# Kernel optimization log

Hardware: AMD Instinct MI355X
Metric: run time of the kernel (lower is better)

Reference implementation:

```python
import jax, jax.numpy as jnp
import numpy as np

K_CODES = 64
EPS_LN = 1e-5


def hamilton_product(p, q):
    # p, q: [..., D] with D = 4*Q, components ordered (r, i, j, k)
    Q = p.shape[-1] // 4
    pr, pi, pj, pk = (p[..., :Q], p[..., Q:2*Q], p[..., 2*Q:3*Q], p[..., 3*Q:])
    qr, qi, qj, qk = (q[..., :Q], q[..., Q:2*Q], q[..., 2*Q:3*Q], q[..., 3*Q:])
    out_r = pr * qr - pi * qi - pj * qj - pk * qk
    out_i = pr * qi + pi * qr + pj * qk - pk * qj
    out_j = pr * qj - pi * qk + pj * qr + pk * qi
    out_k = pr * qk + pi * qj - pj * qi + pk * qr
    return jnp.concatenate([out_r, out_i, out_j, out_k], axis=-1)


def quaternion_linear(x, w4, b):
    # w4: [4, Qo, Qi] stacked (r, i, j, k); builds Hamilton block matrix [D, D]
    r, i, j, k = w4[0], w4[1], w4[2], w4[3]
    W = jnp.block([[r, -i, -j, -k],
                   [i,  r, -k,  j],
                   [j,  k,  r, -i],
                   [k, -j,  i,  r]])
    return x @ W.T + b


def quaternion_layernorm(x, gamma, beta):
    # independent LayerNorm over each quaternion component (4 chunks of size Q)
    Qd = x.shape[-1] // 4
    xs = x.reshape(*x.shape[:-1], 4, Qd)
    mu = xs.mean(axis=-1, keepdims=True)
    var = ((xs - mu) ** 2).mean(axis=-1, keepdims=True)
    xn = (xs - mu) / jnp.sqrt(var + EPS_LN)
    out = xn * gamma + beta  # gamma/beta: [4, Qd]
    return out.reshape(*x.shape[:-1], 4 * Qd)


def setup_inputs() -> dict:
    key = jax.random.key(0)
    ks = jax.random.split(key, 8)
    B, N, D, m = 8, 4096, 512, 3
    Qd = D // 4
    q = jax.random.normal(ks[0], (B, N, D), dtype=jnp.float32)
    assign_idx = jax.random.randint(ks[1], (B, N, m), 0, K_CODES)
    assign_w = jax.random.uniform(ks[2], (B, N, m), dtype=jnp.float32)
    contribute_mask = jnp.ones((B, N), dtype=jnp.float32)
    scale = 0.5 / np.sqrt(Qd)
    proto_w = jax.random.normal(ks[3], (4, Qd, Qd), dtype=jnp.float32) * scale
    proto_b = jax.random.normal(ks[4], (D,), dtype=jnp.float32) * 0.01
    upd_w = jax.random.normal(ks[5], (4, Qd, Qd), dtype=jnp.float32) * scale
    upd_b = jax.random.normal(ks[6], (D,), dtype=jnp.float32) * 0.01
    ln_gamma = jnp.ones((4, Qd), dtype=jnp.float32)
    ln_beta = jnp.zeros((4, Qd), dtype=jnp.float32)
    return {"q": q, "assign_idx": assign_idx, "assign_w": assign_w,
            "contribute_mask": contribute_mask, "proto_w": proto_w,
            "proto_b": proto_b, "upd_w": upd_w, "upd_b": upd_b,
            "ln_gamma": ln_gamma, "ln_beta": ln_beta}


def reference(q, assign_idx, assign_w, contribute_mask, proto_w, proto_b,
              upd_w, upd_b, ln_gamma, ln_beta):
    B, N, D = q.shape
    m = assign_idx.shape[-1]
    K = K_CODES

    # --- scatter-add prototype aggregation ---
    agg_w = assign_w * contribute_mask[..., None]            # [B, N, m]
    flat_idx = assign_idx.reshape(B, N * m)                  # [B, N*m]
    flat_w = agg_w.reshape(B, N * m, 1)                      # [B, N*m, 1]
    weighted_q = (q[:, :, None, :] * agg_w[..., None]).reshape(B, N * m, D)

    seg = lambda v, idx: jax.ops.segment_sum(v, idx, num_segments=K)
    proto = jax.vmap(seg)(weighted_q, flat_idx)              # [B, K, D]
    weight_sum = jax.vmap(seg)(flat_w, flat_idx)             # [B, K, 1]
    proto = proto / (weight_sum + 1e-6)
    proto = quaternion_linear(proto, proto_w, proto_b)       # [B, K, D]

    # --- gather prototypes per observation + Hamilton routing ---
    proto_per_obs = jax.vmap(lambda p, idx: p[idx])(proto, assign_idx)  # [B, N, m, D]
    routed = hamilton_product(q[:, :, None, :], proto_per_obs)          # [B, N, m, D]
    msg = (routed * assign_w[..., None]).sum(axis=2)                    # [B, N, D]
    msg = quaternion_linear(msg, upd_w, upd_b)

    q_new = quaternion_layernorm(q + msg, ln_gamma, ln_beta)
    return q_new, proto
```

## Files before the change

kernel.cpp:

```cpp
#include <hip/hip_runtime.h>
#include <hip/hip_bf16.h>

#define B_ 8
#define N_ 4096
#define D_ 512
#define K_ 64
#define QD_ 128

typedef float f32x4 __attribute__((ext_vector_type(4)));
typedef short short8 __attribute__((ext_vector_type(8)));
typedef unsigned short u16;
typedef unsigned int u32;

__device__ __forceinline__ u16 f2bf(float f) {
  u32 u = __float_as_uint(f);
  return (u16)((u + 0x7fffu + ((u >> 16) & 1u)) >> 16);
}
__device__ __forceinline__ float bf2f(u16 h) {
  return __uint_as_float((u32)h << 16);
}

__device__ __forceinline__ void load8f(const float* p, float* r) {
  float4 a = *(const float4*)(p);
  float4 b = *(const float4*)(p + 4);
  r[0] = a.x; r[1] = a.y; r[2] = a.z; r[3] = a.w;
  r[4] = b.x; r[5] = b.y; r[6] = b.z; r[7] = b.w;
}

__device__ __forceinline__ void store_comp(char* msgL, int row, int u, int s,
                                           int swz, const float* m) {
  uint4 val;
  val.x = (u32)f2bf(m[0]) | ((u32)f2bf(m[1]) << 16);
  val.y = (u32)f2bf(m[2]) | ((u32)f2bf(m[3]) << 16);
  val.z = (u32)f2bf(m[4]) | ((u32)f2bf(m[5]) << 16);
  val.w = (u32)f2bf(m[6]) | ((u32)f2bf(m[7]) << 16);
  const int byte = (row * 1024 + u * 256 + s * 16) ^ swz;
  *(uint4*)(msgL + byte) = val;
}

__global__ __launch_bounds__(256) void k_prep(
    const float* __restrict__ uw, const float* __restrict__ pw,
    u16* __restrict__ uwf, u16* __restrict__ pwf,
    const int* __restrict__ aidx, const float* __restrict__ aw,
    const float* __restrict__ mask, u16* __restrict__ A) {
  if (blockIdx.x < 2048) {
    const int gid = blockIdx.x * 256 + threadIdx.x;
    const int sel = gid >> 18;
    const int idx = gid & ((1 << 18) - 1);
    const int e = idx & 7;
    const int lane = (idx >> 3) & 63;
    const int ks = (idx >> 9) & 15;
    const int cf = idx >> 13;
    const int col = (cf >> 3) * 128 + (cf & 7) * 16 + (lane & 15);
    const int v = ks * 32 + (lane >> 4) * 8 + e;
    const int u = col >> 7, a = col & 127, c = v >> 7, bb = v & 127;
    const int   matT[4][4] = {{0,1,2,3},{1,0,3,2},{2,3,0,1},{3,2,1,0}};
    const float sgnT[4][4] = {{1.f,-1.f,-1.f,-1.f},{1.f,1.f,-1.f,1.f},
                              {1.f,1.f,1.f,-1.f},{1.f,-1.f,1.f,1.f}};
    const float* w4 = sel ? pw : uw;
    u16* dst = sel ? pwf : uwf;
    dst[idx] = f2bf(sgnT[u][c] * w4[matT[u][c] * QD_ * QD_ + a * QD_ + bb]);
  } else {
    const int gid = (blockIdx.x - 2048) * 256 + threadIdx.x;
    const int b = gid >> 12, n = gid & 4095;
    const size_t ib = (size_t)gid * 3;
    const int k0 = aidx[ib], k1 = aidx[ib + 1], k2 = aidx[ib + 2];
    const float mk = mask[gid];
    float w0 = aw[ib] * mk, w1 = aw[ib + 1] * mk, w2 = aw[ib + 2] * mk;
    bool skip1 = false, skip2 = false;
    if (k1 == k0) { w0 += w1; skip1 = true; }
    if (k2 == k0) { w0 += w2; skip2 = true; }
    else if (k2 == k1 && !skip1) { w1 += w2; skip2 = true; }
    u16* Ab = A + (size_t)b * K_ * N_;
#pragma unroll
    for (int k = 0; k < K_; ++k) Ab[(size_t)k * N_ + n] = 0;
    Ab[(size_t)k0 * N_ + n] = f2bf(w0);
    if (!skip1) Ab[(size_t)k1 * N_ + n] = f2bf(w1);
    if (!skip2) Ab[(size_t)k2 * N_ + n] = f2bf(w2);
  }
}

__global__ __launch_bounds__(256) void k_gemmA(
    const u16* __restrict__ A, const float* __restrict__ q,
    float* __restrict__ proto_raw, float* __restrict__ wsum) {
  __shared__ __align__(16) u16 Bt[128 * 64];
  const int t = threadIdx.x;
  const int bid = blockIdx.x;
  const int wg = (bid & 7) * 64 + (bid >> 3);
  const int kc = wg & 15;
  const int dq = (wg >> 4) & 3;
  const int b = wg >> 6;
  const int n_base = kc * 256;
  const u16* Ab = A + (size_t)b * K_ * N_;
  const float* qb = q + ((size_t)b * N_ + n_base) * D_ + dq * 128;

  const int lane = t & 63, wv = t >> 6;
  const int g = lane >> 4, l16 = lane & 15;
  const int sn = t >> 2, sdq = (t & 3) * 32;

  f32x4 acc[4][2];
#pragma unroll
  for (int mt = 0; mt < 4; ++mt)
#pragma unroll
    for (int nt = 0; nt < 2; ++nt) { f32x4 z = {0.f,0.f,0.f,0.f}; acc[mt][nt] = z; }

  float4 pre[8];
#pragma unroll
  for (int e = 0; e < 8; ++e)
    pre[e] = *(const float4*)(qb + (size_t)sn * D_ + sdq + e * 4);

  for (int sub = 0; sub < 4; ++sub) {
    __syncthreads();
#pragma unroll
    for (int e = 0; e < 8; ++e) {
      const float4 v = pre[e];
#pragma unroll
      for (int x = 0; x < 4; ++x) {
        const int d = sdq + e * 4 + x;
        const float fv = (x == 0) ? v.x : (x == 1) ? v.y : (x == 2) ? v.z : v.w;
        const int byte = (d * 128 + sn * 2) ^ ((d & 7) << 4);
        *(u16*)((char*)Bt + byte) = f2bf(fv);
      }
    }
    float4 nxt[8];
    if (sub < 3) {
#pragma unroll
      for (int e = 0; e < 8; ++e)
        nxt[e] = *(const float4*)(qb + (size_t)((sub + 1) * 64 + sn) * D_ + sdq + e * 4);
    }
    __syncthreads();
    const int n0 = n_base + sub * 64;
#pragma unroll
    for (int ks = 0; ks < 2; ++ks) {
      short8 bfrag[2];
#pragma unroll
      for (int nt = 0; nt < 2; ++nt) {
        const int d = wv * 32 + nt * 16 + l16;
        const int byte = (d * 128 + (ks * 32 + g * 8) * 2) ^ ((d & 7) << 4);
        bfrag[nt] = *(const short8*)((const char*)Bt + byte);
      }
#pragma unroll
      for (int mt = 0; mt < 4; ++mt) {
        const short8 afr = *(const short8*)(Ab + (size_t)(mt * 16 + l16) * N_ +
                                            n0 + ks * 32 + g * 8);
#pragma unroll
        for (int nt = 0; nt < 2; ++nt)
          acc[mt][nt] = __builtin_amdgcn_mfma_f32_16x16x32_bf16(afr, bfrag[nt], acc[mt][nt], 0, 0, 0);
      }
    }
#pragma unroll
    for (int e = 0; e < 8; ++e) pre[e] = nxt[e];
  }

#pragma unroll
  for (int mt = 0; mt < 4; ++mt)
#pragma unroll
    for (int nt = 0; nt < 2; ++nt)
#pragma unroll
      for (int rg = 0; rg < 4; ++rg) {
        const int code = mt * 16 + g * 4 + rg;
        const int d = dq * 128 + wv * 32 + nt * 16 + l16;
        atomicAdd(&proto_raw[((size_t)b * K_ + code) * D_ + d], acc[mt][nt][rg]);
      }

  if (dq == 0) {
    const int k = t >> 2, part = t & 3;
    const u16* ap = Ab + (size_t)k * N_ + n_base + part * 64;
    float s = 0.f;
#pragma unroll
    for (int i = 0; i < 8; ++i) {
      const short8 v = *(const short8*)(ap + i * 8);
#pragma unroll
      for (int e = 0; e < 8; ++e) s += bf2f((u16)v[e]);
    }
    s += __shfl_xor(s, 1);
    s += __shfl_xor(s, 2);
    if (part == 0) atomicAdd(&wsum[b * K_ + k], s);
  }
}

__global__ __launch_bounds__(256) void k_proto_mfma(
    const float* __restrict__ proto_raw, const float* __restrict__ wsum,
    const u16* __restrict__ pwf, const float* __restrict__ pb,
    float* __restrict__ proto_t, float* __restrict__ out_proto) {
  __shared__ __align__(16) u16 msgL[16 * 512];
  __shared__ float invs[16];
  const int t = threadIdx.x;
  const size_t R0 = (size_t)blockIdx.x * 16;
  if (t < 16) invs[t] = 1.f / (wsum[R0 + t] + 1e-6f);
  __syncthreads();

  {
    const int s = t & 15, row = t >> 4;
    const float iv = invs[row];
    const float* base = proto_raw + (R0 + row) * D_;
    const int swz = (row & 7) << 4;
#pragma unroll
    for (int u = 0; u < 4; ++u) {
      float m[8];
      load8f(base + u * 128 + s * 8, m);
#pragma unroll
      for (int e = 0; e < 8; ++e) m[e] *= iv;
      store_comp((char*)msgL, row, u, s, swz, m);
    }
  }
  __syncthreads();

  const int lane = t & 63, wv = t >> 6;
  const int g = lane >> 4, l16 = lane & 15;
  f32x4 acc[8];
#pragma unroll
  for (int f = 0; f < 8; ++f) { f32x4 z = {0.f,0.f,0.f,0.f}; acc[f] = z; }
#pragma unroll 4
  for (int ks = 0; ks < 16; ++ks) {
    const int arow = l16;
    const short8 a = *(const short8*)((const char*)msgL +
        ((arow * 1024 + ks * 64 + g * 16) ^ ((arow & 7) << 4)));
#pragma unroll
    for (int f = 0; f < 8; ++f) {
      const short8 bv = *(const short8*)(pwf +
          ((size_t)((wv * 8 + f) * 16 + ks) * 64 + lane) * 8);
      acc[f] = __builtin_amdgcn_mfma_f32_16x16x32_bf16(a, bv, acc[f], 0, 0, 0);
    }
  }

#pragma unroll
  for (int f = 0; f < 8; ++f) {
    const int col = wv * 128 + f * 16 + l16;
    const float pbv = pb[col];
#pragma unroll
    for (int rg = 0; rg < 4; ++rg) {
      const size_t row = R0 + g * 4 + rg;
      const float v = acc[f][rg] + pbv;
      proto_t[row * D_ + col] = v;
      out_proto[row * D_ + col] = v;
    }
  }
}

__global__ __launch_bounds__(256) void k_main8(
    const float* __restrict__ q, const int* __restrict__ aidx,
    const float* __restrict__ aw, const float* __restrict__ proto_t,
    const u16* __restrict__ uwf, const float* __restrict__ ub,
    const float* __restrict__ gamma, const float* __restrict__ beta,
    float* __restrict__ out_q) {
  __shared__ __align__(16) u16 msgL[32 * 512];
  const int t = threadIdx.x;
  const int bid = blockIdx.x;
  const size_t R0 = (size_t)((bid & 7) * 128 + (bid >> 3)) * 32;

  {
    const int s = t & 15, rowHalf = t >> 4;
    int kks[2][3]; float wws[2][3];
#pragma unroll
    for (int p = 0; p < 2; ++p) {
      const size_t gr = R0 + p * 16 + rowHalf;
      const int* ip = aidx + gr * 3;
      const float* wp = aw + gr * 3;
#pragma unroll
      for (int j = 0; j < 3; ++j) { kks[p][j] = ip[j]; wws[p][j] = wp[j]; }
    }
#pragma unroll
    for (int p = 0; p < 2; ++p) {
      const int row = p * 16 + rowHalf;
      const size_t gr = R0 + row;
      const int b = (int)(gr >> 12);
      const float* qp = q + gr * D_ + s * 8;
      float qr_[8], qi_[8], qj_[8], qk_[8];
      load8f(qp, qr_); load8f(qp + 128, qi_);
      load8f(qp + 256, qj_); load8f(qp + 384, qk_);
      float Pr[8], Pi[8], Pj[8], Pk[8];
#pragma unroll
      for (int e = 0; e < 8; ++e) { Pr[e] = Pi[e] = Pj[e] = Pk[e] = 0.f; }
#pragma unroll
      for (int j = 0; j < 3; ++j) {
        const float w = wws[p][j];
        const float* pp = proto_t + (size_t)(b * K_ + kks[p][j]) * D_ + s * 8;
        float pr[8], pi[8], pj[8], pk[8];
        load8f(pp, pr); load8f(pp + 128, pi);
        load8f(pp + 256, pj); load8f(pp + 384, pk);
#pragma unroll
        for (int e = 0; e < 8; ++e) {
          Pr[e] += w * pr[e]; Pi[e] += w * pi[e];
          Pj[e] += w * pj[e]; Pk[e] += w * pk[e];
        }
      }
      const int swz = (row & 7) << 4;
      float m[8];
#pragma unroll
      for (int e = 0; e < 8; ++e)
        m[e] = qr_[e]*Pr[e] - qi_[e]*Pi[e] - qj_[e]*Pj[e] - qk_[e]*Pk[e];
      store_comp((char*)msgL, row, 0, s, swz, m);
#pragma unroll
      for (int e = 0; e < 8; ++e)
        m[e] = qr_[e]*Pi[e] + qi_[e]*Pr[e] + qj_[e]*Pk[e] - qk_[e]*Pj[e];
      store_comp((char*)msgL, row, 1, s, swz, m);
#pragma unroll
      for (int e = 0; e < 8; ++e)
        m[e] = qr_[e]*Pj[e] - qi_[e]*Pk[e] + qj_[e]*Pr[e] + qk_[e]*Pi[e];
      store_comp((char*)msgL, row, 2, s, swz, m);
#pragma unroll
      for (int e = 0; e < 8; ++e)
        m[e] = qr_[e]*Pk[e] + qi_[e]*Pj[e] - qj_[e]*Pi[e] + qk_[e]*Pr[e];
      store_comp((char*)msgL, row, 3, s, swz, m);
    }
  }
  __syncthreads();

  const int lane = t & 63, c4 = t >> 6;
  const int g = lane >> 4, l16 = lane & 15;
  f32x4 acc[2][8];
#pragma unroll
  for (int st = 0; st < 2; ++st)
#pragma unroll
    for (int f = 0; f < 8; ++f) { f32x4 z = {0.f,0.f,0.f,0.f}; acc[st][f] = z; }
#pragma unroll 2
  for (int ks = 0; ks < 16; ++ks) {
    short8 bfr[8];
#pragma unroll
    for (int f = 0; f < 8; ++f)
      bfr[f] = *(const short8*)(uwf +
          ((size_t)((c4 * 8 + f) * 16 + ks) * 64 + lane) * 8);
#pragma unroll
    for (int st = 0; st < 2; ++st) {
      const int arow = st * 16 + l16;
      const short8 a = *(const short8*)((const char*)msgL +
          ((arow * 1024 + ks * 64 + g * 16) ^ ((arow & 7) << 4)));
#pragma unroll
      for (int f = 0; f < 8; ++f)
        acc[st][f] = __builtin_amdgcn_mfma_f32_16x16x32_bf16(a, bfr[f], acc[st][f], 0, 0, 0);
    }
  }

  const int colQ = c4 * 128;
#pragma unroll
  for (int st = 0; st < 2; ++st)
#pragma unroll
    for (int f = 0; f < 8; ++f) {
      const int col = colQ + f * 16 + l16;
      const float ubv = ub[col];
#pragma unroll
      for (int rg = 0; rg < 4; ++rg) {
        const size_t row = R0 + st * 16 + g * 4 + rg;
        acc[st][f][rg] += ubv + q[row * D_ + col];
      }
    }
#pragma unroll
  for (int st = 0; st < 2; ++st)
#pragma unroll
    for (int rg = 0; rg < 4; ++rg) {
      float s = 0.f;
#pragma unroll
      for (int f = 0; f < 8; ++f) s += acc[st][f][rg];
      s += __shfl_xor(s, 1); s += __shfl_xor(s, 2);
      s += __shfl_xor(s, 4); s += __shfl_xor(s, 8);
      const float mean = s * 0.0078125f;
      float sq = 0.f;
#pragma unroll
      for (int f = 0; f < 8; ++f) {
        const float d = acc[st][f][rg] - mean; sq += d * d;
      }
      sq += __shfl_xor(sq, 1); sq += __shfl_xor(sq, 2);
      sq += __shfl_xor(sq, 4); sq += __shfl_xor(sq, 8);
      const float rstd = rsqrtf(sq * 0.0078125f + 1e-5f);
      const size_t row = R0 + st * 16 + g * 4 + rg;
#pragma unroll
      for (int f = 0; f < 8; ++f) {
        const int col = colQ + f * 16 + l16;
        const float xn = (acc[st][f][rg] - mean) * rstd;
        out_q[row * D_ + col] = xn * gamma[col] + beta[col];
      }
    }
}

extern "C" void kernel_launch(void* const* d_in, const int* in_sizes, int n_in,
                              void* d_out, int out_size, void* d_ws, size_t ws_size,
                              hipStream_t stream) {
  const float* q     = (const float*)d_in[0];
  const int*   aidx  = (const int*)d_in[1];
  const float* aw    = (const float*)d_in[2];
  const float* mask  = (const float*)d_in[3];
  const float* pw    = (const float*)d_in[4];
  const float* pb    = (const float*)d_in[5];
  const float* uw    = (const float*)d_in[6];
  const float* ub    = (const float*)d_in[7];
  const float* gamma = (const float*)d_in[8];
  const float* beta  = (const float*)d_in[9];

  char* ws = (char*)d_ws;
  const size_t MB = 1 << 20;
  float* proto_raw = (float*)ws;
  float* wsum      = (float*)(ws + MB);
  u16*   A         = (u16*)(ws + MB + 4096);
  float* proto_t   = (float*)(ws + 5 * MB + 4096);
  u16*   uwf       = (u16*)(ws + 6 * MB + 4096);
  u16*   pwf       = (u16*)(ws + 6 * MB + 4096 + (512 << 10));

  float* out_q = (float*)d_out;
  float* out_proto = out_q + (size_t)B_ * N_ * D_;

  hipMemsetAsync(ws, 0, MB + 4096, stream);
  k_prep<<<2048 + 128, 256, 0, stream>>>(uw, pw, uwf, pwf, aidx, aw, mask, A);
  k_gemmA<<<512, 256, 0, stream>>>(A, q, proto_raw, wsum);
  k_proto_mfma<<<32, 256, 0, stream>>>(proto_raw, wsum, pwf, pb, proto_t, out_proto);
  k_main8<<<1024, 256, 0, stream>>>(q, aidx, aw, proto_t, uwf, ub, gamma, beta, out_q);
}
```

Before: 126.8 us.

## Fuse prototype linear into gemmA via last-block counter, fold memset into prep

Removes the separate hipMemsetAsync by zeroing proto_raw, wsum and new per-batch counters in extra blocks of the prep kernel. Removes the k_proto_mfma launch: each gemmA block increments a per-batch atomic counter after a threadfence, and the last block of each batch normalises and runs the quaternion linear MFMA for that batch's 64 prototypes. This saves two launches and their gaps. The cost is a serialized tail where 8 single blocks each do 4 sequential 16-row groups, instead of 32 parallel blocks.

```diff
diff --git a/kernel.cpp b/kernel.cpp
--- a/kernel.cpp
+++ b/kernel.cpp
@@ -42,7 +42,9 @@
     const float* __restrict__ uw, const float* __restrict__ pw,
     u16* __restrict__ uwf, u16* __restrict__ pwf,
     const int* __restrict__ aidx, const float* __restrict__ aw,
-    const float* __restrict__ mask, u16* __restrict__ A) {
+    const float* __restrict__ mask, u16* __restrict__ A,
+    float* __restrict__ proto_raw, float* __restrict__ wsum,
+    u32* __restrict__ counters) {
   if (blockIdx.x < 2048) {
     const int gid = blockIdx.x * 256 + threadIdx.x;
     const int sel = gid >> 18;
@@ -60,7 +62,7 @@
     const float* w4 = sel ? pw : uw;
     u16* dst = sel ? pwf : uwf;
     dst[idx] = f2bf(sgnT[u][c] * w4[matT[u][c] * QD_ * QD_ + a * QD_ + bb]);
-  } else {
+  } else if (blockIdx.x < 2176) {
     const int gid = (blockIdx.x - 2048) * 256 + threadIdx.x;
     const int b = gid >> 12, n = gid & 4095;
     const size_t ib = (size_t)gid * 3;
@@ -77,12 +79,23 @@
     Ab[(size_t)k0 * N_ + n] = f2bf(w0);
     if (!skip1) Ab[(size_t)k1 * N_ + n] = f2bf(w1);
     if (!skip2) Ab[(size_t)k2 * N_ + n] = f2bf(w2);
+  } else if (blockIdx.x < 2184) {
+    float4 z = {0.f, 0.f, 0.f, 0.f};
+    float4* dst = (float4*)proto_raw + (size_t)(blockIdx.x - 2176) * 8192;
+    for (int i = threadIdx.x; i < 8192; i += 256) dst[i] = z;
+  } else {
+    float4 z = {0.f, 0.f, 0.f, 0.f};
+    if (threadIdx.x < 128) ((float4*)wsum)[threadIdx.x] = z;
+    if (threadIdx.x < 8) counters[threadIdx.x] = 0;
   }
 }
 
 __global__ __launch_bounds__(256) void k_gemmA(
     const u16* __restrict__ A, const float* __restrict__ q,
-    float* __restrict__ proto_raw, float* __restrict__ wsum) {
+    float* __restrict__ proto_raw, float* __restrict__ wsum,
+    u32* __restrict__ counters, const u16* __restrict__ pwf,
+    const float* __restrict__ pb, float* __restrict__ proto_t,
+    float* __restrict__ out_proto) {
   __shared__ __align__(16) u16 Bt[128 * 64];
   const int t = threadIdx.x;
   const int bid = blockIdx.x;
@@ -177,63 +190,59 @@
     s += __shfl_xor(s, 2);
     if (part == 0) atomicAdd(&wsum[b * K_ + k], s);
   }
-}
-
-__global__ __launch_bounds__(256) void k_proto_mfma(
-    const float* __restrict__ proto_raw, const float* __restrict__ wsum,
-    const u16* __restrict__ pwf, const float* __restrict__ pb,
-    float* __restrict__ proto_t, float* __restrict__ out_proto) {
-  __shared__ __align__(16) u16 msgL[16 * 512];
-  __shared__ float invs[16];
-  const int t = threadIdx.x;
-  const size_t R0 = (size_t)blockIdx.x * 16;
-  if (t < 16) invs[t] = 1.f / (wsum[R0 + t] + 1e-6f);
+
+  __threadfence();
+  __shared__ u32 done_s;
+  if (t == 0) done_s = atomicAdd(&counters[b], 1u);
   __syncthreads();
-
-  {
-    const int s = t & 15, row = t >> 4;
-    const float iv = invs[row];
-    const float* base = proto_raw + (R0 + row) * D_;
-    const int swz = (row & 7) << 4;
-#pragma unroll
-    for (int u = 0; u < 4; ++u) {
-      float m[8];
-      load8f(base + u * 128 + s * 8, m);
-#pragma unroll
-      for (int e = 0; e < 8; ++e) m[e] *= iv;
-      store_comp((char*)msgL, row, u, s, swz, m);
-    }
-  }
-  __syncthreads();
-
-  const int lane = t & 63, wv = t >> 6;
-  const int g = lane >> 4, l16 = lane & 15;
-  f32x4 acc[8];
-#pragma unroll
-  for (int f = 0; f < 8; ++f) { f32x4 z = {0.f,0.f,0.f,0.f}; acc[f] = z; }
+  if (done_s == 63) {
+    __threadfence();
+#pragma unroll 1
+    for (int grp = 0; grp < 4; ++grp) {
+      const size_t R0p = (size_t)b * K_ + grp * 16;
+      __syncthreads();
+      {
+        const int s = t & 15, row = t >> 4;
+        const float iv = 1.f / (wsum[R0p + row] + 1e-6f);
+        const float* base = proto_raw + (R0p + row) * D_;
+        const int swz = (row & 7) << 4;
+#pragma unroll
+        for (int u = 0; u < 4; ++u) {
+          float m[8];
+          load8f(base + u * 128 + s * 8, m);
+#pragma unroll
+          for (int e = 0; e < 8; ++e) m[e] *= iv;
+          store_comp((char*)Bt, row, u, s, swz, m);
+        }
+      }
+      __syncthreads();
+      f32x4 pacc[8];
+#pragma unroll
+      for (int f = 0; f < 8; ++f) { f32x4 z = {0.f,0.f,0.f,0.f}; pacc[f] = z; }
 #pragma unroll 4
-  for (int ks = 0; ks < 16; ++ks) {
-    const int arow = l16;
-    const short8 a = *(const short8*)((const char*)msgL +
-        ((arow * 1024 + ks * 64 + g * 16) ^ ((arow & 7) << 4)));
-#pragma unroll
-    for (int f = 0; f < 8; ++f) {
-      const short8 bv = *(const short8*)(pwf +
-          ((size_t)((wv * 8 + f) * 16 + ks) * 64 + lane) * 8);
-      acc[f] = __builtin_amdgcn_mfma_f32_16x16x32_bf16(a, bv, acc[f], 0, 0, 0);
-    }
-  }
-
-#pragma unroll
-  for (int f = 0; f < 8; ++f) {
-    const int col = wv * 128 + f * 16 + l16;
-    const float pbv = pb[col];
-#pragma unroll
-    for (int rg = 0; rg < 4; ++rg) {
-      const size_t row = R0 + g * 4 + rg;
-      const float v = acc[f][rg] + pbv;
-      proto_t[row * D_ + col] = v;
-      out_proto[row * D_ + col] = v;
+      for (int ks = 0; ks < 16; ++ks) {
+        const int arow = l16;
+        const short8 a = *(const short8*)((const char*)Bt +
+            ((arow * 1024 + ks * 64 + g * 16) ^ ((arow & 7) << 4)));
+#pragma unroll
+        for (int f = 0; f < 8; ++f) {
+          const short8 bv = *(const short8*)(pwf +
+              ((size_t)((wv * 8 + f) * 16 + ks) * 64 + lane) * 8);
+          pacc[f] = __builtin_amdgcn_mfma_f32_16x16x32_bf16(a, bv, pacc[f], 0, 0, 0);
+        }
+      }
+#pragma unroll
+      for (int f = 0; f < 8; ++f) {
+        const int col = wv * 128 + f * 16 + l16;
+        const float pbv = pb[col];
+#pragma unroll
+        for (int rg = 0; rg < 4; ++rg) {
+          const size_t row = R0p + g * 4 + rg;
+          const float v = pacc[f][rg] + pbv;
+          proto_t[row * D_ + col] = v;
+          out_proto[row * D_ + col] = v;
+        }
+      }
     }
   }
 }
@@ -391,6 +400,7 @@
   const size_t MB = 1 << 20;
   float* proto_raw = (float*)ws;
   float* wsum      = (float*)(ws + MB);
+  u32*   counters  = (u32*)(ws + MB + 2048);
   u16*   A         = (u16*)(ws + MB + 4096);
   float* proto_t   = (float*)(ws + 5 * MB + 4096);
   u16*   uwf       = (u16*)(ws + 6 * MB + 4096);
@@ -399,9 +409,9 @@
   float* out_q = (float*)d_out;
   float* out_proto = out_q + (size_t)B_ * N_ * D_;
 
-  hipMemsetAsync(ws, 0, MB + 4096, stream);
-  k_prep<<<2048 + 128, 256, 0, stream>>>(uw, pw, uwf, pwf, aidx, aw, mask, A);
-  k_gemmA<<<512, 256, 0, stream>>>(A, q, proto_raw, wsum);
-  k_proto_mfma<<<32, 256, 0, stream>>>(proto_raw, wsum, pwf, pb, proto_t, out_proto);
+  k_prep<<<2185, 256, 0, stream>>>(uw, pw, uwf, pwf, aidx, aw, mask, A,
+                                   proto_raw, wsum, counters);
+  k_gemmA<<<512, 256, 0, stream>>>(A, q, proto_raw, wsum, counters, pwf, pb,
+                                   proto_t, out_proto);
   k_main8<<<1024, 256, 0, stream>>>(q, aidx, aw, proto_t, uwf, ub, gamma, beta, out_q);
 }
```

After: 193.6 us. 52.6% more time.
